# Performance work log

Measured on AMD Instinct MI355X. Metric: run time of the kernel, lower is better.

Reference implementation:

```python
import jax, jax.numpy as jnp
import numpy as np

# dims
B, T, N, D = 4, 256, 64, 512
H, DH = 8, 64            # n_head, d_head; H*DH == D
DF = 4 * D               # SwiGLU hidden
EPS = 1e-6


def rmsnorm(x, w):
    return x * jax.lax.rsqrt(jnp.mean(x * x, axis=-1, keepdims=True) + EPS) * w


def phi(x):
    # positive feature map for kernelized (linear) attention ('SMReg' assumed elu+1 style)
    return jax.nn.elu(x) + 1.0


def heads(x):
    return x.reshape(*x.shape[:-1], H, DH)


def lin_att(Xq, Xkv, wq, wk, wv, wo):
    # low-rank high-order linear attention: kernelized attention applied
    # independently along each tensor mode (time T, entities N), averaged.
    q = phi(heads(Xq @ wq))   # [B,T,N,H,DH]
    k = phi(heads(Xkv @ wk))
    v = heads(Xkv @ wv)
    # mode 1 (time): attend over T, batch over (B,N)
    kv_t = jnp.einsum('btnhk,btnhv->bnhkv', k, v)          # [B,N,H,DH,DH]
    ks_t = k.sum(axis=1)                                   # [B,N,H,DH]
    den_t = jnp.einsum('btnhk,bnhk->btnh', q, ks_t) + EPS
    out_t = jnp.einsum('btnhk,bnhkv->btnhv', q, kv_t) / den_t[..., None]
    # mode 2 (entities): attend over N, batch over (B,T)
    kv_n = jnp.einsum('btnhk,btnhv->bthkv', k, v)
    ks_n = k.sum(axis=2)
    den_n = jnp.einsum('btnhk,bthk->btnh', q, ks_n) + EPS
    out_n = jnp.einsum('btnhk,bthkv->btnhv', q, kv_n) / den_n[..., None]
    out = 0.5 * (out_t + out_n)
    return out.reshape(*Xq.shape[:-1], H * DH) @ wo


def swiglu(x, w1, w2, w3):
    return (jax.nn.silu(x @ w1) * (x @ w3)) @ w2


def setup_inputs() -> dict:
    key = jax.random.key(0)
    ks = jax.random.split(key, 20)
    s = 0.02
    inp = {
        'X': jax.random.normal(ks[0], (B, T, N, D), jnp.float32),
        'Z': jax.random.normal(ks[1], (B, T, N, D), jnp.float32),
        'n1': jnp.ones((D,), jnp.float32),
        'n2': jnp.ones((D,), jnp.float32),
        'n3': jnp.ones((D,), jnp.float32),
        'nz': jnp.ones((D,), jnp.float32),
        'a_wq': jax.random.normal(ks[2], (D, H * DH), jnp.float32) * s,
        'a_wk': jax.random.normal(ks[3], (D, H * DH), jnp.float32) * s,
        'a_wv': jax.random.normal(ks[4], (D, H * DH), jnp.float32) * s,
        'a_wo': jax.random.normal(ks[5], (H * DH, D), jnp.float32) * s,
        'c_wq': jax.random.normal(ks[6], (D, H * DH), jnp.float32) * s,
        'c_wk': jax.random.normal(ks[7], (D, H * DH), jnp.float32) * s,
        'c_wv': jax.random.normal(ks[8], (D, H * DH), jnp.float32) * s,
        'c_wo': jax.random.normal(ks[9], (H * DH, D), jnp.float32) * s,
        'f_w1': jax.random.normal(ks[10], (D, DF), jnp.float32) * s,
        'f_w2': jax.random.normal(ks[11], (DF, D), jnp.float32) * s,
        'f_w3': jax.random.normal(ks[12], (D, DF), jnp.float32) * s,
    }
    return inp


def reference(X, Z, n1, n2, n3, nz, a_wq, a_wk, a_wv, a_wo,
              c_wq, c_wk, c_wv, c_wo, f_w1, f_w2, f_w3):
    # h = X + SelfAtt(norm1(X))
    xn = rmsnorm(X, n1)
    h = X + lin_att(xn, xn, a_wq, a_wk, a_wv, a_wo)
    # h = h + CrossAtt(norm3(h), normz(Z))
    h = h + lin_att(rmsnorm(h, n3), rmsnorm(Z, nz), c_wq, c_wk, c_wv, c_wo)
    # out = h + SwiGLU(norm2(h))   (dropout p=0 -> identity)
    return h + swiglu(rmsnorm(h, n2), f_w1, f_w2, f_w3)
```

## Files before the change

### kernel.cpp

```cpp
#include <hip/hip_runtime.h>

typedef short s16x8 __attribute__((ext_vector_type(8)));
typedef float f32x4 __attribute__((ext_vector_type(4)));
typedef unsigned short u16;
typedef unsigned int u32;

__device__ __forceinline__ float bf2f(u16 u) {
  union { unsigned int i; float f; } v; v.i = ((unsigned int)u) << 16; return v.f;
}
__device__ __forceinline__ u16 f2bf(float f) {
  union { float f; unsigned int i; } v; v.f = f;
  unsigned int r = v.i + 0x7fffu + ((v.i >> 16) & 1u);
  return (u16)(r >> 16);
}
__device__ __forceinline__ float bflo(u32 x) {
  union { unsigned int i; float f; } v; v.i = x << 16; return v.f;
}
__device__ __forceinline__ float bfhi(u32 x) {
  union { unsigned int i; float f; } v; v.i = x & 0xffff0000u; return v.f;
}

__device__ __forceinline__ void gload16(const u16* g, u16* l) {
  __builtin_amdgcn_global_load_lds(
      (const __attribute__((address_space(1))) u32*)g,
      (__attribute__((address_space(3))) u32*)l, 16, 0, 0);
}

template<int KDIM, int NDIM>
__launch_bounds__(256)
__global__ void wprep(const float* __restrict__ in, u16* __restrict__ out) {
  __shared__ float t[64][65];
  const int tid = threadIdx.x;
  const int nb = NDIM / 64;
  const int tk0 = (blockIdx.x / nb) * 64;
  const int tn0 = (blockIdx.x % nb) * 64;
#pragma unroll
  for (int i = 0; i < 16; i++) {
    int idx = i * 256 + tid;
    int r = idx >> 6, c = idx & 63;
    t[r][c] = in[(long)(tk0 + r) * NDIM + (tn0 + c)];
  }
  __syncthreads();
#pragma unroll
  for (int i = 0; i < 16; i++) {
    int idx = i * 256 + tid;
    int nn = idx >> 6, kk = idx & 63;
    out[(long)(tn0 + nn) * KDIM + (tk0 + kk)] = f2bf(t[kk][nn]);
  }
}

__launch_bounds__(256)
__global__ void rmsnorm_f32(const float* __restrict__ x, const float* __restrict__ w,
                            u16* __restrict__ out) {
  const long row = (long)blockIdx.x * 4 + (threadIdx.x >> 6);
  const int lane = threadIdx.x & 63;
  const float* xr = x + row * 512 + lane * 8;
  float4 v0 = *(const float4*)xr;
  float4 v1 = *(const float4*)(xr + 4);
  float ss = v0.x*v0.x + v0.y*v0.y + v0.z*v0.z + v0.w*v0.w
           + v1.x*v1.x + v1.y*v1.y + v1.z*v1.z + v1.w*v1.w;
#pragma unroll
  for (int o = 1; o < 64; o <<= 1) ss += __shfl_xor(ss, o);
  float sc = rsqrtf(ss * (1.0f / 512.0f) + 1e-6f);
  const float* wp = w + lane * 8;
  float4 w0 = *(const float4*)wp;
  float4 w1 = *(const float4*)(wp + 4);
  union { u16 u[8]; uint4 v; } o;
  o.u[0] = f2bf(v0.x * sc * w0.x);
  o.u[1] = f2bf(v0.y * sc * w0.y);
  o.u[2] = f2bf(v0.z * sc * w0.z);
  o.u[3] = f2bf(v0.w * sc * w0.w);
  o.u[4] = f2bf(v1.x * sc * w1.x);
  o.u[5] = f2bf(v1.y * sc * w1.y);
  o.u[6] = f2bf(v1.z * sc * w1.z);
  o.u[7] = f2bf(v1.w * sc * w1.w);
  *(uint4*)(out + row * 512 + lane * 8) = o.v;
}

__launch_bounds__(256)
__global__ void rmsnorm_bf16(const u16* __restrict__ x, const float* __restrict__ w,
                             u16* __restrict__ out) {
  const long row = (long)blockIdx.x * 4 + (threadIdx.x >> 6);
  const int lane = threadIdx.x & 63;
  uint4 u = *(const uint4*)(x + row * 512 + lane * 8);
  const u16* us = (const u16*)&u;
  float f[8];
  float ss = 0.f;
#pragma unroll
  for (int j = 0; j < 8; j++) { f[j] = bf2f(us[j]); ss += f[j] * f[j]; }
#pragma unroll
  for (int o = 1; o < 64; o <<= 1) ss += __shfl_xor(ss, o);
  float sc = rsqrtf(ss * (1.0f / 512.0f) + 1e-6f);
  const float* wp = w + lane * 8;
  union { u16 u[8]; uint4 v; } o;
#pragma unroll
  for (int j = 0; j < 8; j++) o.u[j] = f2bf(f[j] * sc * wp[j]);
  *(uint4*)(out + row * 512 + lane * 8) = o.v;
}

enum { EPI_BF16 = 0, EPI_PHI = 1, EPI_RESX = 2, EPI_RESH = 3, EPI_SILUMUL = 4,
       EPI_OUTF = 5, EPI_QKV = 6, EPI_KV = 7 };

template<int KD, int EPI>
__launch_bounds__(256, 5)
__global__ void gemm128(const u16* __restrict__ A, const u16* __restrict__ Bt,
                        void* __restrict__ C0, void* __restrict__ C1,
                        void* __restrict__ C2, const void* __restrict__ aux,
                        int Ns) {
  __shared__ u16 smem[16384];
  const int tid = threadIdx.x;
  const int lane = tid & 63;
  const int wv = tid >> 6;
  const int gx = gridDim.x;
  int L = blockIdx.y * gx + blockIdx.x;
  const int cpx = (gx * gridDim.y) >> 3;
  L = (L & 7) * cpx + (L >> 3);
  const long m0 = (long)(L / gx) * 128;
  const int nb = L % gx;
  const long n0 = (long)nb * 128;

  const int wr = (wv >> 1) * 64;
  const int wc = (wv & 1) * 64;
  const int fr = lane & 15;
  const int frq = lane >> 4;

  const int sig = (lane & 7) ^ ((lane >> 3) & 7);
  const int grow = wv * 32 + 2 * (lane >> 3) + (sig >> 2);
  const u16* Ag = A + (m0 + grow) * KD + (sig & 3) * 8;
  const u16* Bg = Bt + (n0 + grow) * KD + (sig & 3) * 8;

  f32x4 acc[4][4] = {};

  auto STAGE = [&](int b, int kt) {
    const long k0 = (long)kt * 32;
    gload16(Ag + k0, smem + b * 4096 + wv * 1024);
    gload16(Ag + (long)16 * KD + k0, smem + b * 4096 + wv * 1024 + 512);
    gload16(Bg + k0, smem + 8192 + b * 4096 + wv * 1024);
    gload16(Bg + (long)16 * KD + k0, smem + 8192 + b * 4096 + wv * 1024 + 512);
  };
  auto COMPUTE = [&](int b) {
    s16x8 af[4], bf[4];
#pragma unroll
    for (int i = 0; i < 4; i++) {
      const int r = wr + i * 16 + fr;
      const int pr = r >> 1;
      const int sl = (((r & 1) * 4 + frq) ^ (pr & 7)) * 8;
      af[i] = *(const s16x8*)&smem[b * 4096 + pr * 64 + sl];
    }
#pragma unroll
    for (int j = 0; j < 4; j++) {
      const int r = wc + j * 16 + fr;
      const int pr = r >> 1;
      const int sl = (((r & 1) * 4 + frq) ^ (pr & 7)) * 8;
      bf[j] = *(const s16x8*)&smem[8192 + b * 4096 + pr * 64 + sl];
    }
#pragma unroll
    for (int i = 0; i < 4; i++)
#pragma unroll
      for (int j = 0; j < 4; j++)
        acc[i][j] = __builtin_amdgcn_mfma_f32_16x16x32_bf16(af[i], bf[j], acc[i][j], 0, 0, 0);
  };

  constexpr int NT = KD / 32;
  STAGE(0, 0);
#pragma unroll 1
  for (int t = 0; t < NT; ++t) {
    if (t + 1 < NT) {
      STAGE((t + 1) & 1, t + 1);
      asm volatile("s_waitcnt vmcnt(4)" ::: "memory");
    } else {
      asm volatile("s_waitcnt vmcnt(0)" ::: "memory");
    }
    __builtin_amdgcn_s_barrier();
    COMPUTE(t & 1);
    asm volatile("s_waitcnt lgkmcnt(0)" ::: "memory");
    __builtin_amdgcn_s_barrier();
  }

  u16* Cs = smem;
  const int col = lane & 15;
  const int rb = frq * 4;
  const int seg = (EPI == EPI_QKV || EPI == EPI_KV) ? (nb >> 2) : 0;
#pragma unroll
  for (int hh = 0; hh < 2; ++hh) {
    if ((wv >> 1) == hh) {
#pragma unroll
      for (int i = 0; i < 4; i++) {
#pragma unroll
        for (int r = 0; r < 4; r++) {
          const int mloc = i * 16 + rb + r;
#pragma unroll
          for (int j = 0; j < 4; j++) {
            const int nl = wc + j * 16 + col;
            float v = acc[i][j][r];
            if constexpr (EPI == EPI_PHI) {
              v = v > 0.f ? v + 1.f : __expf(v);
            } else if constexpr (EPI == EPI_QKV) {
              if (seg < 2) v = v > 0.f ? v + 1.f : __expf(v);
            } else if constexpr (EPI == EPI_KV) {
              if (seg == 0) v = v > 0.f ? v + 1.f : __expf(v);
            }
            Cs[mloc * 132 + nl] = f2bf(v);
          }
        }
      }
    }
    __syncthreads();
#pragma unroll
    for (int rep = 0; rep < 4; rep++) {
      const int idx = rep * 256 + tid;
      const int row = idx >> 4;
      const int nc = (idx & 15) * 8;
      const long m = m0 + hh * 64 + row;
      uint4 vv = *(const uint4*)&Cs[row * 132 + nc];
      const u16* vp = (const u16*)&vv;
      if constexpr (EPI == EPI_QKV) {
        u16* P = (u16*)(seg == 0 ? C0 : (seg == 1 ? C1 : C2));
        *(uint4*)(P + m * 512 + (int)((n0 + nc) & 511)) = vv;
      } else if constexpr (EPI == EPI_KV) {
        u16* P = (u16*)(seg == 0 ? C0 : C1);
        *(uint4*)(P + m * 512 + (int)((n0 + nc) & 511)) = vv;
      } else if constexpr (EPI == EPI_BF16 || EPI == EPI_PHI) {
        *(uint4*)((u16*)C0 + m * Ns + n0 + nc) = vv;
      } else if constexpr (EPI == EPI_RESX) {
        const float* ax = (const float*)aux + m * Ns + n0 + nc;
        float4 a0 = *(const float4*)ax;
        float4 a1 = *(const float4*)(ax + 4);
        union { u16 u[8]; uint4 v; } o;
        o.u[0] = f2bf(a0.x + bf2f(vp[0]));
        o.u[1] = f2bf(a0.y + bf2f(vp[1]));
        o.u[2] = f2bf(a0.z + bf2f(vp[2]));
        o.u[3] = f2bf(a0.w + bf2f(vp[3]));
        o.u[4] = f2bf(a1.x + bf2f(vp[4]));
        o.u[5] = f2bf(a1.y + bf2f(vp[5]));
        o.u[6] = f2bf(a1.z + bf2f(vp[6]));
        o.u[7] = f2bf(a1.w + bf2f(vp[7]));
        *(uint4*)((u16*)C0 + m * Ns + n0 + nc) = o.v;
      } else if constexpr (EPI == EPI_RESH) {
        uint4 hhv = *(const uint4*)((const u16*)aux + m * Ns + n0 + nc);
        const u16* hp = (const u16*)&hhv;
        union { u16 u[8]; uint4 v; } o;
#pragma unroll
        for (int e = 0; e < 8; e++) o.u[e] = f2bf(bf2f(hp[e]) + bf2f(vp[e]));
        *(uint4*)((u16*)C0 + m * Ns + n0 + nc) = o.v;
      } else if constexpr (EPI == EPI_SILUMUL) {
        uint4 tt = *(const uint4*)((const u16*)aux + m * Ns + n0 + nc);
        const u16* tp = (const u16*)&tt;
        union { u16 u[8]; uint4 v; } o;
#pragma unroll
        for (int e = 0; e < 8; e++) {
          float t2 = bf2f(tp[e]);
          float s = t2 / (1.f + __expf(-t2));
          o.u[e] = f2bf(s * bf2f(vp[e]));
        }
        *(uint4*)((u16*)C0 + m * Ns + n0 + nc) = o.v;
      } else {
        uint4 hhv = *(const uint4*)((const u16*)aux + m * Ns + n0 + nc);
        const u16* hp = (const u16*)&hhv;
        float* o = (float*)C0 + m * Ns + n0 + nc;
        float4 o0, o1;
        o0.x = bf2f(hp[0]) + bf2f(vp[0]);
        o0.y = bf2f(hp[1]) + bf2f(vp[1]);
        o0.z = bf2f(hp[2]) + bf2f(vp[2]);
        o0.w = bf2f(hp[3]) + bf2f(vp[3]);
        o1.x = bf2f(hp[4]) + bf2f(vp[4]);
        o1.y = bf2f(hp[5]) + bf2f(vp[5]);
        o1.z = bf2f(hp[6]) + bf2f(vp[6]);
        o1.w = bf2f(hp[7]) + bf2f(vp[7]);
        *(float4*)o = o0;
        *(float4*)(o + 4) = o1;
      }
    }
    if (hh == 0) __syncthreads();
  }
}

__launch_bounds__(256)
__global__ void att_mode1(const u16* __restrict__ q, const u16* __restrict__ k,
                          const u16* __restrict__ v, u16* __restrict__ attc) {
  __shared__ u32 KT[64][132];
  __shared__ u32 VT[64][132];
  __shared__ u16 KVT[64][72];
  __shared__ float ksump[4][64];
  __shared__ float ksum_s[64];
  __shared__ float dinv[256];
  const int tid = threadIdx.x;
  const int lane = tid & 63;
  const int w = tid >> 6;
  const int bnh = blockIdx.x;
  const int h = bnh & 7;
  const int bn = bnh >> 3;
  const int n = bn & 63;
  const int b = bn >> 6;
  const long base = ((long)b * 16384 + n) * 512 + h * 64;
  const int fr = lane & 15;
  const int frq = lane >> 4;
  const int fk = frq * 8;

#pragma unroll
  for (int r = 0; r < 4; r++) {
    const int tp = (tid & 63) + (r & 1) * 64;
    const int c8 = (tid >> 6) + (r >> 1) * 4;
    const long g0 = base + (long)(2 * tp) * 32768 + c8 * 8;
    uint4 ka = *(const uint4*)(k + g0);
    uint4 kb = *(const uint4*)(k + g0 + 32768);
    uint4 va = *(const uint4*)(v + g0);
    uint4 vb = *(const uint4*)(v + g0 + 32768);
    const u16* kap = (const u16*)&ka; const u16* kbp = (const u16*)&kb;
    const u16* vap = (const u16*)&va; const u16* vbp = (const u16*)&vb;
#pragma unroll
    for (int e = 0; e < 8; e++) {
      KT[c8 * 8 + e][tp] = (u32)kap[e] | ((u32)kbp[e] << 16);
      VT[c8 * 8 + e][tp] = (u32)vap[e] | ((u32)vbp[e] << 16);
    }
  }
  __syncthreads();

  {
    const int dk = tid >> 2, qq = tid & 3;
    float s = 0.f;
#pragma unroll
    for (int i = 0; i < 8; i++) {
      uint4 x = *(const uint4*)&KT[dk][qq * 32 + i * 4];
      s += bflo(x.x) + bfhi(x.x) + bflo(x.y) + bfhi(x.y)
         + bflo(x.z) + bfhi(x.z) + bflo(x.w) + bfhi(x.w);
    }
    ksump[qq][dk] = s;
  }

  f32x4 acc[4] = {};
#pragma unroll
  for (int ks = 0; ks < 8; ks++) {
    s16x8 af = *(const s16x8*)&VT[w * 16 + fr][ks * 16 + frq * 4];
    s16x8 bk[4];
#pragma unroll
    for (int j = 0; j < 4; j++)
      bk[j] = *(const s16x8*)&KT[j * 16 + fr][ks * 16 + frq * 4];
#pragma unroll
    for (int j = 0; j < 4; j++)
      acc[j] = __builtin_amdgcn_mfma_f32_16x16x32_bf16(af, bk[j], acc[j], 0, 0, 0);
  }
  __syncthreads();
  {
    const int colL = lane & 15, rb = frq * 4;
#pragma unroll
    for (int j = 0; j < 4; j++)
#pragma unroll
      for (int r = 0; r < 4; r++)
        KVT[w * 16 + rb + r][j * 16 + colL] = f2bf(acc[j][r]);
  }
  if (tid < 64) ksum_s[tid] = ksump[0][tid] + ksump[1][tid] + ksump[2][tid] + ksump[3][tid];
  __syncthreads();
  {
    const u16* qp = q + base + (long)tid * 32768;
    float d = 0.f;
#pragma unroll
    for (int c8 = 0; c8 < 8; c8++) {
      uint4 u = ((const uint4*)qp)[c8];
      const u16* us = (const u16*)&u;
#pragma unroll
      for (int e = 0; e < 8; e++) d += bf2f(us[e]) * ksum_s[c8 * 8 + e];
    }
    dinv[tid] = 0.5f / (d + 1e-6f);
  }
  f32x4 acc2[4][4] = {};
#pragma unroll
  for (int ks = 0; ks < 2; ks++) {
    s16x8 aq[4], bk[4];
#pragma unroll
    for (int i = 0; i < 4; i++)
      aq[i] = *(const s16x8*)(q + base + (long)(w * 64 + i * 16 + fr) * 32768 + ks * 32 + fk);
#pragma unroll
    for (int j = 0; j < 4; j++)
      bk[j] = *(const s16x8*)&KVT[j * 16 + fr][ks * 32 + fk];
#pragma unroll
    for (int i = 0; i < 4; i++)
#pragma unroll
      for (int j = 0; j < 4; j++)
        acc2[i][j] = __builtin_amdgcn_mfma_f32_16x16x32_bf16(aq[i], bk[j], acc2[i][j], 0, 0, 0);
  }
  __syncthreads();
  const int colL = lane & 15, rb = frq * 4;
#pragma unroll
  for (int i = 0; i < 4; i++)
#pragma unroll
    for (int r = 0; r < 4; r++) {
      int t = w * 64 + i * 16 + rb + r;
      float inv = dinv[t];
#pragma unroll
      for (int j = 0; j < 4; j++)
        attc[base + (long)t * 32768 + j * 16 + colL] = f2bf(acc2[i][j][r] * inv);
    }
}

__launch_bounds__(256)
__global__ void att_mode2(const u16* __restrict__ q, const u16* __restrict__ k,
                          const u16* __restrict__ v, u16* __restrict__ attc) {
  __shared__ u32 KT[64][36];
  __shared__ u32 VT[64][36];
  __shared__ u16 KVT[64][72];
  __shared__ float ksump[4][64];
  __shared__ float ksum_s[64];
  __shared__ float dinv[64];
  const int tid = threadIdx.x;
  const int lane = tid & 63;
  const int w = tid >> 6;
  const int bth = blockIdx.x;
  const int h = bth & 7;
  const long bt = bth >> 3;
  const long base = bt * 32768 + h * 64;
  const int fr = lane & 15;
  const int frq = lane >> 4;
  const int fk = frq * 8;

  {
    const int np = tid & 31;
    const int c8 = tid >> 5;
    const long g0 = base + (long)(2 * np) * 512 + c8 * 8;
    uint4 ka = *(const uint4*)(k + g0);
    uint4 kb = *(const uint4*)(k + g0 + 512);
    uint4 va = *(const uint4*)(v + g0);
    uint4 vb = *(const uint4*)(v + g0 + 512);
    const u16* kap = (const u16*)&ka; const u16* kbp = (const u16*)&kb;
    const u16* vap = (const u16*)&va; const u16* vbp = (const u16*)&vb;
#pragma unroll
    for (int e = 0; e < 8; e++) {
      KT[c8 * 8 + e][np] = (u32)kap[e] | ((u32)kbp[e] << 16);
      VT[c8 * 8 + e][np] = (u32)vap[e] | ((u32)vbp[e] << 16);
    }
  }
  __syncthreads();
  {
    const int dk = tid >> 2, qq = tid & 3;
    uint4 x0 = *(const uint4*)&KT[dk][qq * 8];
    uint4 x1 = *(const uint4*)&KT[dk][qq * 8 + 4];
    float s = bflo(x0.x) + bfhi(x0.x) + bflo(x0.y) + bfhi(x0.y)
            + bflo(x0.z) + bfhi(x0.z) + bflo(x0.w) + bfhi(x0.w)
            + bflo(x1.x) + bfhi(x1.x) + bflo(x1.y) + bfhi(x1.y)
            + bflo(x1.z) + bfhi(x1.z) + bflo(x1.w) + bfhi(x1.w);
    ksump[qq][dk] = s;
  }
  f32x4 acc[4] = {};
#pragma unroll
  for (int ks = 0; ks < 2; ks++) {
    s16x8 af = *(const s16x8*)&VT[w * 16 + fr][ks * 16 + frq * 4];
    s16x8 bk[4];
#pragma unroll
    for (int j = 0; j < 4; j++)
      bk[j] = *(const s16x8*)&KT[j * 16 + fr][ks * 16 + frq * 4];
#pragma unroll
    for (int j = 0; j < 4; j++)
      acc[j] = __builtin_amdgcn_mfma_f32_16x16x32_bf16(af, bk[j], acc[j], 0, 0, 0);
  }
  __syncthreads();
  {
    const int colL = lane & 15, rb = frq * 4;
#pragma unroll
    for (int j = 0; j < 4; j++)
#pragma unroll
      for (int r = 0; r < 4; r++)
        KVT[w * 16 + rb + r][j * 16 + colL] = f2bf(acc[j][r]);
  }
  if (tid < 64) ksum_s[tid] = ksump[0][tid] + ksump[1][tid] + ksump[2][tid] + ksump[3][tid];
  __syncthreads();
  if (tid < 64) {
    const u16* qp = q + base + (long)tid * 512;
    float d = 0.f;
#pragma unroll
    for (int c8 = 0; c8 < 8; c8++) {
      uint4 u = ((const uint4*)qp)[c8];
      const u16* us = (const u16*)&u;
#pragma unroll
      for (int e = 0; e < 8; e++) d += bf2f(us[e]) * ksum_s[c8 * 8 + e];
    }
    dinv[tid] = 0.5f / (d + 1e-6f);
  }
  f32x4 acc2[4] = {};
#pragma unroll
  for (int ks = 0; ks < 2; ks++) {
    s16x8 aq, bk[4];
    aq = *(const s16x8*)(q + base + (long)(w * 16 + fr) * 512 + ks * 32 + fk);
#pragma unroll
    for (int j = 0; j < 4; j++)
      bk[j] = *(const s16x8*)&KVT[j * 16 + fr][ks * 32 + fk];
#pragma unroll
    for (int j = 0; j < 4; j++)
      acc2[j] = __builtin_amdgcn_mfma_f32_16x16x32_bf16(aq, bk[j], acc2[j], 0, 0, 0);
  }
  __syncthreads();
  const int colL = lane & 15, rb = frq * 4;
#pragma unroll
  for (int r = 0; r < 4; r++) {
    int nr = w * 16 + rb + r;
    float inv = dinv[nr];
#pragma unroll
    for (int j = 0; j < 4; j++) {
      long o = base + (long)nr * 512 + j * 16 + colL;
      attc[o] = f2bf(bf2f(attc[o]) + acc2[j][r] * inv);
    }
  }
}

extern "C" void kernel_launch(void* const* d_in, const int* in_sizes, int n_in,
                              void* d_out, int out_size, void* d_ws, size_t ws_size,
                              hipStream_t stream) {
  const float* X    = (const float*)d_in[0];
  const float* Z    = (const float*)d_in[1];
  const float* n1   = (const float*)d_in[2];
  const float* n2   = (const float*)d_in[3];
  const float* n3   = (const float*)d_in[4];
  const float* nz   = (const float*)d_in[5];
  const float* a_wq = (const float*)d_in[6];
  const float* a_wk = (const float*)d_in[7];
  const float* a_wv = (const float*)d_in[8];
  const float* a_wo = (const float*)d_in[9];
  const float* c_wq = (const float*)d_in[10];
  const float* c_wk = (const float*)d_in[11];
  const float* c_wv = (const float*)d_in[12];
  const float* c_wo = (const float*)d_in[13];
  const float* f_w1 = (const float*)d_in[14];
  const float* f_w2 = (const float*)d_in[15];
  const float* f_w3 = (const float*)d_in[16];
  float* out = (float*)d_out;
  (void)ws_size; (void)in_sizes; (void)n_in; (void)out_size;

  char* p = (char*)d_ws;
  size_t off = 0;
  auto take = [&](size_t bytes) -> char* {
    char* r = p + off;
    off += (bytes + 255) & ~(size_t)255;
    return r;
  };
  u16* w_aq = (u16*)take(512 * 512 * 2);
  u16* w_ak = (u16*)take(512 * 512 * 2);
  u16* w_av = (u16*)take(512 * 512 * 2);
  u16* w_ao = (u16*)take(512 * 512 * 2);
  u16* w_cq = (u16*)take(512 * 512 * 2);
  u16* w_ck = (u16*)take(512 * 512 * 2);
  u16* w_cv = (u16*)take(512 * 512 * 2);
  u16* w_co = (u16*)take(512 * 512 * 2);
  u16* w_f1 = (u16*)take(2048 * 512 * 2);
  u16* w_f3 = (u16*)take(2048 * 512 * 2);
  u16* w_f2 = (u16*)take(512 * 2048 * 2);
  u16* xn   = (u16*)take((size_t)65536 * 512 * 2);
  u16* hbuf = (u16*)take((size_t)65536 * 512 * 2);
  u16* qbuf = (u16*)take((size_t)65536 * 512 * 2);
  u16* kbuf = (u16*)d_out;
  u16* vbuf = (u16*)d_out + (size_t)65536 * 512;
  u16* attc = xn;
  u16* tslot = qbuf;

  dim3 b256(256);
  dim3 gQKV(12, 512);
  dim3 gKV(8, 512);
  dim3 gP(4, 512);
  dim3 gU(16, 128);
  dim3 gD(4, 128);

  wprep<512, 512><<<64, b256, 0, stream>>>(a_wq, w_aq);
  wprep<512, 512><<<64, b256, 0, stream>>>(a_wk, w_ak);
  wprep<512, 512><<<64, b256, 0, stream>>>(a_wv, w_av);
  wprep<512, 512><<<64, b256, 0, stream>>>(a_wo, w_ao);
  wprep<512, 512><<<64, b256, 0, stream>>>(c_wq, w_cq);
  wprep<512, 512><<<64, b256, 0, stream>>>(c_wk, w_ck);
  wprep<512, 512><<<64, b256, 0, stream>>>(c_wv, w_cv);
  wprep<512, 512><<<64, b256, 0, stream>>>(c_wo, w_co);
  wprep<512, 2048><<<256, b256, 0, stream>>>(f_w1, w_f1);
  wprep<512, 2048><<<256, b256, 0, stream>>>(f_w3, w_f3);
  wprep<2048, 512><<<256, b256, 0, stream>>>(f_w2, w_f2);

  rmsnorm_f32<<<16384, b256, 0, stream>>>(X, n1, xn);
  gemm128<512, EPI_QKV><<<gQKV, b256, 0, stream>>>(xn, w_aq, qbuf, kbuf, vbuf, nullptr, 1536);
  att_mode1<<<2048, b256, 0, stream>>>(qbuf, kbuf, vbuf, attc);
  att_mode2<<<8192, b256, 0, stream>>>(qbuf, kbuf, vbuf, attc);
  gemm128<512, EPI_RESX><<<gP, b256, 0, stream>>>(attc, w_ao, hbuf, nullptr, nullptr, X, 512);

  rmsnorm_bf16<<<16384, b256, 0, stream>>>(hbuf, n3, xn);
  gemm128<512, EPI_PHI><<<gP, b256, 0, stream>>>(xn, w_cq, qbuf, nullptr, nullptr, nullptr, 512);
  rmsnorm_f32<<<16384, b256, 0, stream>>>(Z, nz, xn);
  gemm128<512, EPI_KV><<<gKV, b256, 0, stream>>>(xn, w_ck, kbuf, vbuf, nullptr, nullptr, 1024);
  att_mode1<<<2048, b256, 0, stream>>>(qbuf, kbuf, vbuf, attc);
  att_mode2<<<8192, b256, 0, stream>>>(qbuf, kbuf, vbuf, attc);
  gemm128<512, EPI_RESH><<<gP, b256, 0, stream>>>(attc, w_co, hbuf, nullptr, nullptr, hbuf, 512);

  rmsnorm_bf16<<<16384, b256, 0, stream>>>(hbuf, n2, xn);
  const int CH = 16384;
  for (int c = 0; c < 4; c++) {
    const size_t ro = (size_t)c * CH * 512;
    gemm128<512, EPI_BF16><<<gU, b256, 0, stream>>>(xn + ro, w_f1, tslot, nullptr, nullptr, nullptr, 2048);
    gemm128<512, EPI_SILUMUL><<<gU, b256, 0, stream>>>(xn + ro, w_f3, tslot, nullptr, nullptr, tslot, 2048);
    gemm128<2048, EPI_OUTF><<<gD, b256, 0, stream>>>(tslot, w_f2, out + ro, nullptr, nullptr, hbuf + ro, 512);
  }
}
```

Measured before the change: 1.544 ms.

## Add K=64 double-buffered GEMM for the FFN down-projection and MFMA priority hints

Renames the existing K=32-step GEMM to gemm32 and wraps its MFMA block in s_setprio raises. Adds a new gemm128 that stages 64-wide K tiles into a 64 KB LDS double buffer with an XOR-swizzled layout and does two MFMA sub-steps per tile. Only the K=2048 down-projection uses the new kernel. The aim is fewer barriers and loop iterations per K and better latency hiding, at the cost of more LDS per block and therefore lower occupancy.

```diff
diff --git a/kernel.cpp b/kernel.cpp
--- a/kernel.cpp
+++ b/kernel.cpp
@@ -103,10 +103,10 @@
 
 template<int KD, int EPI>
 __launch_bounds__(256, 5)
-__global__ void gemm128(const u16* __restrict__ A, const u16* __restrict__ Bt,
-                        void* __restrict__ C0, void* __restrict__ C1,
-                        void* __restrict__ C2, const void* __restrict__ aux,
-                        int Ns) {
+__global__ void gemm32(const u16* __restrict__ A, const u16* __restrict__ Bt,
+                       void* __restrict__ C0, void* __restrict__ C1,
+                       void* __restrict__ C2, const void* __restrict__ aux,
+                       int Ns) {
   __shared__ u16 smem[16384];
   const int tid = threadIdx.x;
   const int lane = tid & 63;
@@ -154,11 +154,13 @@
       const int sl = (((r & 1) * 4 + frq) ^ (pr & 7)) * 8;
       bf[j] = *(const s16x8*)&smem[8192 + b * 4096 + pr * 64 + sl];
     }
+    __builtin_amdgcn_s_setprio(1);
 #pragma unroll
     for (int i = 0; i < 4; i++)
 #pragma unroll
       for (int j = 0; j < 4; j++)
         acc[i][j] = __builtin_amdgcn_mfma_f32_16x16x32_bf16(af[i], bf[j], acc[i][j], 0, 0, 0);
+    __builtin_amdgcn_s_setprio(0);
   };
 
   constexpr int NT = KD / 32;
@@ -275,6 +277,168 @@
   }
 }
 
+template<int KD, int EPI>
+__launch_bounds__(256)
+__global__ void gemm128(const u16* __restrict__ A, const u16* __restrict__ Bt,
+                        void* __restrict__ C0, void* __restrict__ C1,
+                        void* __restrict__ C2, const void* __restrict__ aux,
+                        int Ns) {
+  __shared__ u16 smem[32768];
+  u16* Asm = smem;
+  u16* Bsm = smem + 16384;
+  const int tid = threadIdx.x;
+  const int lane = tid & 63;
+  const int wv = tid >> 6;
+  const int gx = gridDim.x;
+  int L = blockIdx.y * gx + blockIdx.x;
+  const int cpx = (gx * gridDim.y) >> 3;
+  L = (L & 7) * cpx + (L >> 3);
+  const long m0 = (long)(L / gx) * 128;
+  const int nb = L % gx;
+  const long n0 = (long)nb * 128;
+
+  const int wr = (wv >> 1) * 64;
+  const int wc = (wv & 1) * 64;
+  const int fr = lane & 15;
+  const int frq = lane >> 4;
+
+  const int r0 = wv * 32 + (lane >> 3);
+  const int sg8 = ((lane & 7) ^ ((lane >> 3) & 7)) * 8;
+  const u16* Ag = A + (m0 + r0) * KD + sg8;
+  const u16* Bg = Bt + (n0 + r0) * KD + sg8;
+  u16* Alds = Asm + wv * 2048;
+  u16* Blds = Bsm + wv * 2048;
+
+  f32x4 acc[4][4] = {};
+
+  auto STAGE = [&](int b, int kt) {
+    const long k0 = (long)kt * 64;
+#pragma unroll
+    for (int j = 0; j < 4; j++) {
+      gload16(Ag + (long)(j * 8) * KD + k0, Alds + b * 8192 + j * 512);
+      gload16(Bg + (long)(j * 8) * KD + k0, Blds + b * 8192 + j * 512);
+    }
+  };
+  auto COMPUTE = [&](int b) {
+#pragma unroll
+    for (int ks = 0; ks < 2; ks++) {
+      const int slot = ((ks * 4 + frq) ^ (fr & 7)) * 8;
+      s16x8 af[4], bf[4];
+#pragma unroll
+      for (int i = 0; i < 4; i++)
+        af[i] = *(const s16x8*)&Asm[b * 8192 + (wr + i * 16 + fr) * 64 + slot];
+#pragma unroll
+      for (int j = 0; j < 4; j++)
+        bf[j] = *(const s16x8*)&Bsm[b * 8192 + (wc + j * 16 + fr) * 64 + slot];
+      __builtin_amdgcn_s_setprio(1);
+#pragma unroll
+      for (int i = 0; i < 4; i++)
+#pragma unroll
+        for (int j = 0; j < 4; j++)
+          acc[i][j] = __builtin_amdgcn_mfma_f32_16x16x32_bf16(af[i], bf[j], acc[i][j], 0, 0, 0);
+      __builtin_amdgcn_s_setprio(0);
+    }
+  };
+
+  constexpr int NT = KD / 64;
+  STAGE(0, 0);
+#pragma unroll 1
+  for (int t = 0; t < NT; ++t) {
+    if (t + 1 < NT) {
+      STAGE((t + 1) & 1, t + 1);
+      asm volatile("s_waitcnt vmcnt(8)" ::: "memory");
+    } else {
+      asm volatile("s_waitcnt vmcnt(0)" ::: "memory");
+    }
+    __builtin_amdgcn_s_barrier();
+    COMPUTE(t & 1);
+    asm volatile("s_waitcnt lgkmcnt(0)" ::: "memory");
+    __builtin_amdgcn_s_barrier();
+  }
+
+  u16* Cs = smem;
+  const int col = lane & 15;
+  const int rb = frq * 4;
+  const int seg = 0; (void)seg;
+#pragma unroll
+  for (int i = 0; i < 4; i++) {
+#pragma unroll
+    for (int r = 0; r < 4; r++) {
+      const int ml = wr + i * 16 + rb + r;
+#pragma unroll
+      for (int j = 0; j < 4; j++) {
+        const int nl = wc + j * 16 + col;
+        float v = acc[i][j][r];
+        if constexpr (EPI == EPI_PHI) {
+          v = v > 0.f ? v + 1.f : __expf(v);
+        }
+        Cs[ml * 148 + nl] = f2bf(v);
+      }
+    }
+  }
+  __syncthreads();
+
+#pragma unroll
+  for (int rep = 0; rep < 8; rep++) {
+    const int idx = rep * 256 + tid;
+    const int row = idx >> 4;
+    const int nc = (idx & 15) * 8;
+    const long m = m0 + row;
+    uint4 vv = *(const uint4*)&Cs[row * 148 + nc];
+    const u16* vp = (const u16*)&vv;
+    if constexpr (EPI == EPI_BF16 || EPI == EPI_PHI) {
+      *(uint4*)((u16*)C0 + m * Ns + n0 + nc) = vv;
+    } else if constexpr (EPI == EPI_RESX) {
+      const float* ax = (const float*)aux + m * Ns + n0 + nc;
+      float4 a0 = *(const float4*)ax;
+      float4 a1 = *(const float4*)(ax + 4);
+      union { u16 u[8]; uint4 v; } o;
+      o.u[0] = f2bf(a0.x + bf2f(vp[0]));
+      o.u[1] = f2bf(a0.y + bf2f(vp[1]));
+      o.u[2] = f2bf(a0.z + bf2f(vp[2]));
+      o.u[3] = f2bf(a0.w + bf2f(vp[3]));
+      o.u[4] = f2bf(a1.x + bf2f(vp[4]));
+      o.u[5] = f2bf(a1.y + bf2f(vp[5]));
+      o.u[6] = f2bf(a1.z + bf2f(vp[6]));
+      o.u[7] = f2bf(a1.w + bf2f(vp[7]));
+      *(uint4*)((u16*)C0 + m * Ns + n0 + nc) = o.v;
+    } else if constexpr (EPI == EPI_RESH) {
+      uint4 hh = *(const uint4*)((const u16*)aux + m * Ns + n0 + nc);
+      const u16* hp = (const u16*)&hh;
+      union { u16 u[8]; uint4 v; } o;
+#pragma unroll
+      for (int e = 0; e < 8; e++) o.u[e] = f2bf(bf2f(hp[e]) + bf2f(vp[e]));
+      *(uint4*)((u16*)C0 + m * Ns + n0 + nc) = o.v;
+    } else if constexpr (EPI == EPI_SILUMUL) {
+      uint4 tt = *(const uint4*)((const u16*)aux + m * Ns + n0 + nc);
+      const u16* tp = (const u16*)&tt;
+      union { u16 u[8]; uint4 v; } o;
+#pragma unroll
+      for (int e = 0; e < 8; e++) {
+        float t2 = bf2f(tp[e]);
+        float s = t2 / (1.f + __expf(-t2));
+        o.u[e] = f2bf(s * bf2f(vp[e]));
+      }
+      *(uint4*)((u16*)C0 + m * Ns + n0 + nc) = o.v;
+    } else {
+      uint4 hh = *(const uint4*)((const u16*)aux + m * Ns + n0 + nc);
+      const u16* hp = (const u16*)&hh;
+      float* o = (float*)C0 + m * Ns + n0 + nc;
+      float4 o0, o1;
+      o0.x = bf2f(hp[0]) + bf2f(vp[0]);
+      o0.y = bf2f(hp[1]) + bf2f(vp[1]);
+      o0.z = bf2f(hp[2]) + bf2f(vp[2]);
+      o0.w = bf2f(hp[3]) + bf2f(vp[3]);
+      o1.x = bf2f(hp[4]) + bf2f(vp[4]);
+      o1.y = bf2f(hp[5]) + bf2f(vp[5]);
+      o1.z = bf2f(hp[6]) + bf2f(vp[6]);
+      o1.w = bf2f(hp[7]) + bf2f(vp[7]);
+      *(float4*)o = o0;
+      *(float4*)(o + 4) = o1;
+    }
+  }
+}
+
 __launch_bounds__(256)
 __global__ void att_mode1(const u16* __restrict__ q, const u16* __restrict__ k,
                           const u16* __restrict__ v, u16* __restrict__ attc) {
@@ -570,25 +734,25 @@
   wprep<2048, 512><<<256, b256, 0, stream>>>(f_w2, w_f2);
 
   rmsnorm_f32<<<16384, b256, 0, stream>>>(X, n1, xn);
-  gemm128<512, EPI_QKV><<<gQKV, b256, 0, stream>>>(xn, w_aq, qbuf, kbuf, vbuf, nullptr, 1536);
+  gemm32<512, EPI_QKV><<<gQKV, b256, 0, stream>>>(xn, w_aq, qbuf, kbuf, vbuf, nullptr, 1536);
   att_mode1<<<2048, b256, 0, stream>>>(qbuf, kbuf, vbuf, attc);
   att_mode2<<<8192, b256, 0, stream>>>(qbuf, kbuf, vbuf, attc);
-  gemm128<512, EPI_RESX><<<gP, b256, 0, stream>>>(attc, w_ao, hbuf, nullptr, nullptr, X, 512);
+  gemm32<512, EPI_RESX><<<gP, b256, 0, stream>>>(attc, w_ao, hbuf, nullptr, nullptr, X, 512);
 
   rmsnorm_bf16<<<16384, b256, 0, stream>>>(hbuf, n3, xn);
-  gemm128<512, EPI_PHI><<<gP, b256, 0, stream>>>(xn, w_cq, qbuf, nullptr, nullptr, nullptr, 512);
+  gemm32<512, EPI_PHI><<<gP, b256, 0, stream>>>(xn, w_cq, qbuf, nullptr, nullptr, nullptr, 512);
   rmsnorm_f32<<<16384, b256, 0, stream>>>(Z, nz, xn);
-  gemm128<512, EPI_KV><<<gKV, b256, 0, stream>>>(xn, w_ck, kbuf, vbuf, nullptr, nullptr, 1024);
+  gemm32<512, EPI_KV><<<gKV, b256, 0, stream>>>(xn, w_ck, kbuf, vbuf, nullptr, nullptr, 1024);
   att_mode1<<<2048, b256, 0, stream>>>(qbuf, kbuf, vbuf, attc);
   att_mode2<<<8192, b256, 0, stream>>>(qbuf, kbuf, vbuf, attc);
-  gemm128<512, EPI_RESH><<<gP, b256, 0, stream>>>(attc, w_co, hbuf, nullptr, nullptr, hbuf, 512);
+  gemm32<512, EPI_RESH><<<gP, b256, 0, stream>>>(attc, w_co, hbuf, nullptr, nullptr, hbuf, 512);
 
   rmsnorm_bf16<<<16384, b256, 0, stream>>>(hbuf, n2, xn);
   const int CH = 16384;
   for (int c = 0; c < 4; c++) {
     const size_t ro = (size_t)c * CH * 512;
-    gemm128<512, EPI_BF16><<<gU, b256, 0, stream>>>(xn + ro, w_f1, tslot, nullptr, nullptr, nullptr, 2048);
-    gemm128<512, EPI_SILUMUL><<<gU, b256, 0, stream>>>(xn + ro, w_f3, tslot, nullptr, nullptr, tslot, 2048);
+    gemm32<512, EPI_BF16><<<gU, b256, 0, stream>>>(xn + ro, w_f1, tslot, nullptr, nullptr, nullptr, 2048);
+    gemm32<512, EPI_SILUMUL><<<gU, b256, 0, stream>>>(xn + ro, w_f3, tslot, nullptr, nullptr, tslot, 2048);
     gemm128<2048, EPI_OUTF><<<gD, b256, 0, stream>>>(tslot, w_f2, out + ro, nullptr, nullptr, hbuf + ro, 512);
   }
 }
```

Measured after the change: 2.263 ms. 46.6% more time.
